# Kernel tuning notes

Measured on AMD Instinct MI355X. Metric: run time of the kernel, lower is better.

## Reference

```python
import jax, jax.numpy as jnp
import numpy as np

BATCH, DIN, HID = 32768, 64, 1024


def setup_inputs() -> dict:
    key = jax.random.key(0)
    ks = jax.random.split(key, 8)
    s_in = 1.0 / np.sqrt(DIN)
    s_h = 1.0 / np.sqrt(HID)
    return {
        "z": jax.random.normal(ks[0], (BATCH, DIN), dtype=jnp.float32),
        # Hamiltonian net: DIN -> HID -> HID -> 1
        "W1": jax.random.normal(ks[1], (DIN, HID), dtype=jnp.float32) * s_in,
        "b1": jnp.zeros((HID,), jnp.float32),
        "W2": jax.random.normal(ks[2], (HID, HID), dtype=jnp.float32) * s_h,
        "b2": jnp.zeros((HID,), jnp.float32),
        "W3": jax.random.normal(ks[3], (HID, 1), dtype=jnp.float32) * s_h,
        "b3": jnp.zeros((1,), jnp.float32),
        # Forcing net: DIN -> HID -> DIN
        "Wf1": jax.random.normal(ks[4], (DIN, HID), dtype=jnp.float32) * s_in,
        "bf1": jnp.zeros((HID,), jnp.float32),
        "Wf2": jax.random.normal(ks[5], (HID, DIN), dtype=jnp.float32) * s_h,
        "bf2": jnp.zeros((DIN,), jnp.float32),
    }


def reference(z, W1, b1, W2, b2, W3, b3, Wf1, bf1, Wf2, bf2):
    def H_sum(zz):
        h1 = jnp.tanh(zz @ W1 + b1)          # [B, HID]
        h2 = jnp.tanh(h1 @ W2 + b2)          # [B, HID]
        return jnp.sum(h2 @ W3 + b3)         # scalar (sum of H over batch)

    gradH = jax.grad(H_sum)(z)               # [B, DIN]
    dim = z.shape[1] // 2
    # symplectic combine: dq/dt = dH/dp, dp/dt = -dH/dq
    hnn_term = jnp.concatenate([gradH[:, dim:], -gradH[:, :dim]], axis=-1)
    forcing_term = jnp.tanh(z @ Wf1 + bf1) @ Wf2 + bf2  # [B, DIN]
    return hnn_term + forcing_term
```

## Files before the change

kernel.cpp:

```cpp
#include <hip/hip_runtime.h>


typedef __attribute__((ext_vector_type(8))) short s16x8;
typedef __attribute__((ext_vector_type(4))) float f32x4;
typedef unsigned short u16;

#define DEVFN static __device__ __forceinline__

constexpr int DIN = 64;
constexpr int HID = 1024;

DEVFN u16 f2bf(float f) {
  unsigned u = __builtin_bit_cast(unsigned, f);
  u += 0x7fffu + ((u >> 16) & 1u);
  return (u16)(u >> 16);
}
DEVFN float bf2f(u16 h) {
  unsigned u = ((unsigned)h) << 16;
  return __builtin_bit_cast(float, u);
}
DEVFN float fast_tanh(float x) {
  float e = __builtin_amdgcn_exp2f(x * 2.8853900817779268f);
  return 1.0f - 2.0f * __builtin_amdgcn_rcpf(e + 1.0f);
}
DEVFN f32x4 mfma16(s16x8 a, s16x8 b, f32x4 c) {
  return __builtin_amdgcn_mfma_f32_16x16x32_bf16(a, b, c, 0, 0, 0);
}

#define GLOAD16(g, l) __builtin_amdgcn_global_load_lds( \
    (const __attribute__((address_space(1))) unsigned int*)(const void*)(g), \
    (__attribute__((address_space(3))) unsigned int*)(void*)(l), 16, 0, 0)

__global__ __launch_bounds__(256) void k0_prep(
    const float* __restrict__ W2, const float* __restrict__ W1,
    const float* __restrict__ Wf1, const float* __restrict__ Wf2,
    u16* __restrict__ W2tp, u16* __restrict__ W2c,
    u16* __restrict__ W1p, u16* __restrict__ Wf1p,
    u16* __restrict__ W1s, u16* __restrict__ Wf2p) {
  __shared__ u16 tl[64 * 65];
  const int bi = blockIdx.x >> 4, bj = blockIdx.x & 15;
  const int tid = threadIdx.x;
#pragma unroll
  for (int i = 0; i < 16; ++i) {
    int idx = i * 256 + tid;
    int r = idx >> 6, c = idx & 63;
    float v = W2[(size_t)(bi * 64 + r) * 1024 + bj * 64 + c];
    u16 b = f2bf(v);
    W2c[(size_t)(bi * 64 + r) * 1024 + bj * 64 + c] = b;
    tl[r * 65 + c] = b;
  }
  __syncthreads();
#pragma unroll
  for (int i = 0; i < 16; ++i) {
    int idx = i * 256 + tid;
    int r = idx >> 6, c = idx & 63;
    W2tp[(size_t)(bj * 64 + r) * 1024 + bi * 64 + c] = tl[c * 65 + r];
  }
  int id = blockIdx.x * 256 + tid;
  int n = id >> 6, k = id & 63;
  W1p[id]  = f2bf(W1[k * HID + n]);
  Wf1p[id] = f2bf(Wf1[k * HID + n]);
  int nn = id >> 10, kk2 = id & 1023;
  float s = (nn < 32) ? 1.f : -1.f;
  W1s[id]  = f2bf(s * W1[((nn + 32) & 63) * HID + kk2]);
  Wf2p[id] = f2bf(Wf2[kk2 * DIN + nn]);
}

__global__ __launch_bounds__(256) void k1_h1(const float* z, const u16* Wp,
                                             const float* b, u16* o) {
  __shared__ __align__(16) u16 zl[64 * 72];
  const int tid = threadIdx.x;
  const int lane = tid & 63, w = tid >> 6;
  const int nb = blockIdx.x & 7, mb = blockIdx.x >> 3;
  const size_t m0 = (size_t)mb * 64;
  const int n0 = nb * 128;
#pragma unroll
  for (int c = 0; c < 4; ++c) {
    int i4 = c * 256 + tid;
    int row = i4 >> 4, col4 = (i4 & 15) * 4;
    f32x4 v = *reinterpret_cast<const f32x4*>(z + (m0 + row) * DIN + col4);
    u16* d = zl + row * 72 + col4;
    d[0] = f2bf(v[0]); d[1] = f2bf(v[1]); d[2] = f2bf(v[2]); d[3] = f2bf(v[3]);
  }
  __syncthreads();
  f32x4 acc[8] = {};
#pragma unroll
  for (int kk = 0; kk < 2; ++kk) {
    const int karr = kk * 32 + ((lane >> 4) << 3);
    s16x8 a = *reinterpret_cast<const s16x8*>(zl + (16 * w + (lane & 15)) * 72 + karr);
#pragma unroll
    for (int fn = 0; fn < 8; ++fn) {
      int n = n0 + fn * 16 + (lane & 15);
      s16x8 bb = *reinterpret_cast<const s16x8*>(Wp + (size_t)n * 64 + karr);
      acc[fn] = mfma16(a, bb, acc[fn]);
    }
  }
#pragma unroll
  for (int fn = 0; fn < 8; ++fn) {
    int n = n0 + fn * 16 + (lane & 15);
    float bias = b[n];
#pragma unroll
    for (int j = 0; j < 4; ++j) {
      size_t m = m0 + 16 * w + ((lane >> 4) << 2) + j;
      o[m * HID + n] = f2bf(fast_tanh(acc[fn][j] + bias));
    }
  }
}

template <int MODE>
__global__ __launch_bounds__(512, 2) void k23_gemm(
    const u16* __restrict__ A, const u16* __restrict__ Bp,
    const float* __restrict__ b2, const float* __restrict__ W3,
    const u16* __restrict__ h1in, u16* __restrict__ outb) {
  extern __shared__ u16 lds[];
  const int tid = threadIdx.x;
  const int lane = tid & 63, w = tid >> 6;
  const int wr = w >> 2, wc = w & 3;
  const int xcd = blockIdx.x & 7, local = blockIdx.x >> 3;
  const size_t m0 = (size_t)(xcd * 16 + (local >> 2)) * 256;
  const int n0 = (local & 3) * 256;

  const u16* gpa[4]; const u16* gpb[4]; int lo[4];
#pragma unroll
  for (int c = 0; c < 4; ++c) {
    int idx = c * 512 + tid, row = idx >> 3, cg = idx & 7;
    int sc = (cg ^ (row & 7)) << 3;
    gpa[c] = A + (m0 + row) * 1024 + sc;
    gpb[c] = Bp + (size_t)(n0 + row) * 1024 + sc;
    lo[c] = idx * 8;
  }
#define STAGE_A(B_, T_) { _Pragma("unroll") for (int c = 0; c < 4; ++c) \
    GLOAD16(gpa[c] + (T_) * 64, lds + (B_) * 32768 + lo[c]); }
#define STAGE_B(B_, T_) { _Pragma("unroll") for (int c = 0; c < 4; ++c) \
    GLOAD16(gpb[c] + (T_) * 64, lds + (B_) * 32768 + 16384 + lo[c]); }

  const int swz = (lane & 7) << 3;
  int aoff[8], boff[4];
#pragma unroll
  for (int i = 0; i < 8; ++i)
    aoff[i] = (wr * 128 + i * 16 + (lane & 15)) * 64 + ((lane >> 4) << 3);
#pragma unroll
  for (int j = 0; j < 4; ++j)
    boff[j] = (wc * 64 + j * 16 + (lane & 15)) * 64 + ((lane >> 4) << 3);

  f32x4 acc[8][4] = {};

#define PHASE(B_, KK_) { \
    s16x8 af[8], bf[4]; \
    _Pragma("unroll") for (int i = 0; i < 8; ++i) \
      af[i] = *reinterpret_cast<const s16x8*>(lds + (B_) * 32768 + ((aoff[i] + (KK_) * 32) ^ swz)); \
    _Pragma("unroll") for (int j = 0; j < 4; ++j) \
      bf[j] = *reinterpret_cast<const s16x8*>(lds + (B_) * 32768 + 16384 + ((boff[j] + (KK_) * 32) ^ swz)); \
    __builtin_amdgcn_s_setprio(1); \
    _Pragma("unroll") for (int i = 0; i < 8; ++i) { \
      _Pragma("unroll") for (int j = 0; j < 4; ++j) \
        acc[i][j] = mfma16(af[i], bf[j], acc[i][j]); } \
    __builtin_amdgcn_s_setprio(0); }

  STAGE_A(0, 0); STAGE_B(0, 0);
  for (int t = 0; t < 15; ++t) {
    const int cur = t & 1, nxt = cur ^ 1;
    STAGE_A(nxt, t + 1);
    asm volatile("s_waitcnt vmcnt(4)" ::: "memory");
    __builtin_amdgcn_s_barrier();
    asm volatile("" ::: "memory");
    PHASE(cur, 0);
    STAGE_B(nxt, t + 1);
    PHASE(cur, 1);
    asm volatile("" ::: "memory");
    __builtin_amdgcn_s_barrier();
    asm volatile("" ::: "memory");
  }
  asm volatile("s_waitcnt vmcnt(0)" ::: "memory");
  __builtin_amdgcn_s_barrier();
  asm volatile("" ::: "memory");
  PHASE(1, 0);
  PHASE(1, 1);
  asm volatile("" ::: "memory");
  __builtin_amdgcn_s_barrier();
  asm volatile("" ::: "memory");

  const int wbase = w * 8192;
  float b2v[4], w3v[4];
  if (MODE == 0) {
#pragma unroll
    for (int j = 0; j < 4; ++j) {
      int n = n0 + wc * 64 + j * 16 + (lane & 15);
      b2v[j] = b2[n]; w3v[j] = W3[n];
    }
  }
#pragma unroll
  for (int h = 0; h < 2; ++h) {
    if (h == 1) asm volatile("s_waitcnt lgkmcnt(0)" ::: "memory");
#pragma unroll
    for (int ip = 0; ip < 4; ++ip) {
#pragma unroll
      for (int j = 0; j < 4; ++j) {
#pragma unroll
        for (int r = 0; r < 4; ++r) {
          float v = acc[h * 4 + ip][j][r];
          u16 o;
          if (MODE == 0) {
            float tt = fast_tanh(v + b2v[j]);
            o = f2bf(w3v[j] * (1.f - tt * tt));
          } else {
            o = f2bf(v);
          }
          int lr = ip * 16 + ((lane >> 4) << 2) + r;
          lds[wbase + lr * 64 + j * 16 + (lane & 15)] = o;
        }
      }
    }
#pragma unroll
    for (int r8 = 0; r8 < 8; ++r8) {
      int lr = r8 * 8 + (lane >> 3), c8 = (lane & 7) * 8;
      s16x8 vv = *reinterpret_cast<const s16x8*>(lds + wbase + lr * 64 + c8);
      size_t grow = m0 + wr * 128 + h * 64 + lr;
      int gcol = n0 + wc * 64 + c8;
      if (MODE == 1) {
        s16x8 hh = *reinterpret_cast<const s16x8*>(h1in + grow * 1024 + gcol);
#pragma unroll
        for (int e = 0; e < 8; ++e) {
          float hv = bf2f((u16)hh[e]);
          vv[e] = (short)f2bf(bf2f((u16)vv[e]) * (1.f - hv * hv));
        }
      }
      *reinterpret_cast<s16x8*>(outb + grow * 1024 + gcol) = vv;
    }
  }
#undef STAGE_A
#undef STAGE_B
#undef PHASE
}

__global__ __launch_bounds__(512) void k4_gemm(
    const u16* __restrict__ gp1, const u16* __restrict__ f1,
    const u16* __restrict__ W1s, const u16* __restrict__ Wf2p,
    const float* __restrict__ bf2, float* __restrict__ out) {
  __shared__ __align__(16) u16 Ab[2][2][4096];
  __shared__ __align__(16) u16 Bb[2][2][4096];
  const int tid = threadIdx.x;
  const int w8 = tid >> 6, lane = tid & 63;
  const int grp = w8 >> 2, w = w8 & 3;
  const int gt = tid & 255;
  const int lr = lane & 15, g = lane >> 4;
  const size_t m0 = (size_t)blockIdx.x * 64;
  const u16* asrc = grp ? f1 : gp1;
  const u16* bsrc = grp ? Wf2p : W1s;

  int aoffs[2], boffs[2], lo[2];
#pragma unroll
  for (int c = 0; c < 2; ++c) {
    int idx = c * 256 + gt;
    int row = idx >> 3, cg = idx & 7;
    aoffs[c] = (int)((m0 + row) * 1024) + ((cg ^ (row & 7)) << 3);
    boffs[c] = row * 1024 + ((cg ^ (row & 7)) << 3);
    lo[c] = idx * 8;
  }
#define K4STAGE(B_, T_) { const int ko_ = (T_) * 64; \
    _Pragma("unroll") for (int c = 0; c < 2; ++c) { \
      GLOAD16(asrc + aoffs[c] + ko_, Ab[grp][B_] + lo[c]); \
      GLOAD16(bsrc + boffs[c] + ko_, Bb[grp][B_] + lo[c]); } }

  const int arow = w * 16 + lr;
  int afr[2], bfr[2][4];
#pragma unroll
  for (int kkl = 0; kkl < 2; ++kkl) {
    afr[kkl] = arow * 64 + ((kkl * 32 + g * 8) ^ ((arow & 7) << 3));
#pragma unroll
    for (int fn = 0; fn < 4; ++fn) {
      int br = fn * 16 + lr;
      bfr[kkl][fn] = br * 64 + ((kkl * 32 + g * 8) ^ ((br & 7) << 3));
    }
  }

  f32x4 acc[4] = {};
#define K4MM(BUF_) { \
    _Pragma("unroll") for (int kkl = 0; kkl < 2; ++kkl) { \
      s16x8 a = *reinterpret_cast<const s16x8*>(Ab[grp][BUF_] + afr[kkl]); \
      _Pragma("unroll") for (int fn = 0; fn < 4; ++fn) { \
        s16x8 b = *reinterpret_cast<const s16x8*>(Bb[grp][BUF_] + bfr[kkl][fn]); \
        acc[fn] = mfma16(a, b, acc[fn]); } } }
#define TBAR() { asm volatile("" ::: "memory"); __builtin_amdgcn_s_barrier(); asm volatile("" ::: "memory"); }

  K4STAGE(0, 0);
  for (int t = 0; t < 15; ++t) {
    K4STAGE((t + 1) & 1, t + 1);
    asm volatile("s_waitcnt vmcnt(4)" ::: "memory");
    TBAR();
    K4MM(t & 1);
    TBAR();
  }
  asm volatile("s_waitcnt vmcnt(0)" ::: "memory");
  TBAR();
  K4MM(1);

  __syncthreads();
  float* red = (float*)&Ab[0][0][0];
  if (grp == 1) {
#pragma unroll
    for (int fn = 0; fn < 4; ++fn)
#pragma unroll
      for (int j = 0; j < 4; ++j)
        red[(fn * 4 + j) * 256 + gt] = acc[fn][j];
  }
  __syncthreads();
  if (grp == 0) {
#pragma unroll
    for (int fn = 0; fn < 4; ++fn) {
      int n = fn * 16 + lr;
      float bias = bf2[n];
#pragma unroll
      for (int j = 0; j < 4; ++j) {
        float v = acc[fn][j] + red[(fn * 4 + j) * 256 + gt] + bias;
        size_t m = m0 + w * 16 + g * 4 + j;
        out[m * DIN + n] = v;
      }
    }
  }
#undef K4STAGE
#undef K4MM
#undef TBAR
}

extern "C" void kernel_launch(void* const* d_in, const int* in_sizes, int n_in,
                              void* d_out, int out_size, void* d_ws, size_t ws_size,
                              hipStream_t stream) {
  const float* z   = (const float*)d_in[0];
  const float* W1  = (const float*)d_in[1];
  const float* b1  = (const float*)d_in[2];
  const float* W2  = (const float*)d_in[3];
  const float* b2  = (const float*)d_in[4];
  const float* W3  = (const float*)d_in[5];
  const float* Wf1 = (const float*)d_in[7];
  const float* bf1 = (const float*)d_in[8];
  const float* Wf2 = (const float*)d_in[9];
  const float* bf2 = (const float*)d_in[10];

  char* ws = (char*)d_ws;
  u16* W1p  = (u16*)(ws + 0);
  u16* Wf1p = (u16*)(ws + 131072);
  u16* W2tp = (u16*)(ws + 262144);
  u16* W2c  = (u16*)(ws + 2359296);
  u16* W1s  = (u16*)(ws + 4456448);
  u16* Wf2p = (u16*)(ws + 4587520);
  u16* h1   = (u16*)(ws + 4718592);
  u16* gp2  = (u16*)(ws + 4718592 + 67108864ull);
  float* out = (float*)d_out;

  k0_prep<<<256, 256, 0, stream>>>(W2, W1, Wf1, Wf2, W2tp, W2c, W1p, Wf1p, W1s, Wf2p);
  k1_h1<<<4096, 256, 0, stream>>>(z, W1p, b1, h1);
  k23_gemm<0><<<512, 512, 131072, stream>>>(h1, W2tp, b2, W3, nullptr, gp2);
  k23_gemm<1><<<512, 512, 131072, stream>>>(gp2, W2c, nullptr, nullptr, h1, h1);
  k1_h1<<<4096, 256, 0, stream>>>(z, Wf1p, bf1, gp2);
  k4_gemm<<<512, 512, 0, stream>>>(h1, gp2, W1s, Wf2p, bf2, out);
}
```

Measured before the change: 251.3 us.

## Split GEMM main loop into four barrier-separated sub-phases with staggered loads

Restructures the double-buffered GEMM main loop into four sub-phases per K-step. Each sub-phase reads half of the A fragments plus the B fragments, issues a quarter of the next tile's global-to-LDS loads, and runs 16 MFMAs, with extra barriers in between. This halves the A-fragment register footprint, which frees registers, and interleaves loads more finely with compute in a ping-pong style schedule. In exchange it roughly triples the number of barriers per iteration, which can stall waves if they are not balanced.

```diff
diff --git a/kernel.cpp b/kernel.cpp
--- a/kernel.cpp
+++ b/kernel.cpp
@@ -129,10 +129,14 @@
     gpb[c] = Bp + (size_t)(n0 + row) * 1024 + sc;
     lo[c] = idx * 8;
   }
-#define STAGE_A(B_, T_) { _Pragma("unroll") for (int c = 0; c < 4; ++c) \
-    GLOAD16(gpa[c] + (T_) * 64, lds + (B_) * 32768 + lo[c]); }
-#define STAGE_B(B_, T_) { _Pragma("unroll") for (int c = 0; c < 4; ++c) \
-    GLOAD16(gpb[c] + (T_) * 64, lds + (B_) * 32768 + 16384 + lo[c]); }
+#define STAGE_H(B_, T_, H_) { \
+    if ((H_) < 2) { \
+      GLOAD16(gpa[(H_) * 2]     + (T_) * 64, lds + (B_) * 32768 + lo[(H_) * 2]); \
+      GLOAD16(gpa[(H_) * 2 + 1] + (T_) * 64, lds + (B_) * 32768 + lo[(H_) * 2 + 1]); \
+    } else { \
+      GLOAD16(gpb[((H_) - 2) * 2]     + (T_) * 64, lds + (B_) * 32768 + 16384 + lo[((H_) - 2) * 2]); \
+      GLOAD16(gpb[((H_) - 2) * 2 + 1] + (T_) * 64, lds + (B_) * 32768 + 16384 + lo[((H_) - 2) * 2 + 1]); \
+    } }
 
   const int swz = (lane & 7) << 3;
   int aoff[8], boff[4];
@@ -144,41 +148,58 @@
     boff[j] = (wc * 64 + j * 16 + (lane & 15)) * 64 + ((lane >> 4) << 3);
 
   f32x4 acc[8][4] = {};
-
-#define PHASE(B_, KK_) { \
-    s16x8 af[8], bf[4]; \
-    _Pragma("unroll") for (int i = 0; i < 8; ++i) \
-      af[i] = *reinterpret_cast<const s16x8*>(lds + (B_) * 32768 + ((aoff[i] + (KK_) * 32) ^ swz)); \
-    _Pragma("unroll") for (int j = 0; j < 4; ++j) \
-      bf[j] = *reinterpret_cast<const s16x8*>(lds + (B_) * 32768 + 16384 + ((boff[j] + (KK_) * 32) ^ swz)); \
-    __builtin_amdgcn_s_setprio(1); \
-    _Pragma("unroll") for (int i = 0; i < 8; ++i) { \
+  s16x8 af[4], bf[4];
+
+#define RDB(B_, KK_) { _Pragma("unroll") for (int j = 0; j < 4; ++j) \
+    bf[j] = *reinterpret_cast<const s16x8*>(lds + (B_) * 32768 + 16384 + ((boff[j] + (KK_) * 32) ^ swz)); }
+#define RDA(B_, MH_, KK_) { _Pragma("unroll") for (int i = 0; i < 4; ++i) \
+    af[i] = *reinterpret_cast<const s16x8*>(lds + (B_) * 32768 + ((aoff[(MH_) * 4 + i] + (KK_) * 32) ^ swz)); }
+#define MM16(MH_) { __builtin_amdgcn_s_setprio(1); \
+    _Pragma("unroll") for (int i = 0; i < 4; ++i) { \
       _Pragma("unroll") for (int j = 0; j < 4; ++j) \
-        acc[i][j] = mfma16(af[i], bf[j], acc[i][j]); } \
+        acc[(MH_) * 4 + i][j] = mfma16(af[i], bf[j], acc[(MH_) * 4 + i][j]); } \
     __builtin_amdgcn_s_setprio(0); }
-
-  STAGE_A(0, 0); STAGE_B(0, 0);
+#define BAR() { asm volatile("" ::: "memory"); __builtin_amdgcn_s_barrier(); asm volatile("" ::: "memory"); }
+
+  STAGE_H(0, 0, 0); STAGE_H(0, 0, 1); STAGE_H(0, 0, 2); STAGE_H(0, 0, 3);
   for (int t = 0; t < 15; ++t) {
     const int cur = t & 1, nxt = cur ^ 1;
-    STAGE_A(nxt, t + 1);
-    asm volatile("s_waitcnt vmcnt(4)" ::: "memory");
-    __builtin_amdgcn_s_barrier();
-    asm volatile("" ::: "memory");
-    PHASE(cur, 0);
-    STAGE_B(nxt, t + 1);
-    PHASE(cur, 1);
-    asm volatile("" ::: "memory");
-    __builtin_amdgcn_s_barrier();
-    asm volatile("" ::: "memory");
+    STAGE_H(nxt, t + 1, 0);
+    asm volatile("s_waitcnt vmcnt(2)" ::: "memory");
+    BAR();
+    RDB(cur, 0); RDA(cur, 0, 0);
+    MM16(0);
+    BAR();
+    RDA(cur, 1, 0);
+    STAGE_H(nxt, t + 1, 1);
+    BAR();
+    MM16(1);
+    BAR();
+    RDB(cur, 1); RDA(cur, 0, 1);
+    STAGE_H(nxt, t + 1, 2);
+    BAR();
+    MM16(0);
+    BAR();
+    RDA(cur, 1, 1);
+    STAGE_H(nxt, t + 1, 3);
+    BAR();
+    MM16(1);
+    BAR();
   }
   asm volatile("s_waitcnt vmcnt(0)" ::: "memory");
-  __builtin_amdgcn_s_barrier();
-  asm volatile("" ::: "memory");
-  PHASE(1, 0);
-  PHASE(1, 1);
-  asm volatile("" ::: "memory");
-  __builtin_amdgcn_s_barrier();
-  asm volatile("" ::: "memory");
+  BAR();
+  RDB(1, 0); RDA(1, 0, 0);
+  MM16(0);
+  BAR();
+  RDA(1, 1, 0);
+  MM16(1);
+  BAR();
+  RDB(1, 1); RDA(1, 0, 1);
+  MM16(0);
+  BAR();
+  RDA(1, 1, 1);
+  MM16(1);
+  BAR();
 
   const int wbase = w * 8192;
   float b2v[4], w3v[4];
@@ -228,9 +249,11 @@
       *reinterpret_cast<s16x8*>(outb + grow * 1024 + gcol) = vv;
     }
   }
-#undef STAGE_A
-#undef STAGE_B
-#undef PHASE
+#undef STAGE_H
+#undef RDB
+#undef RDA
+#undef MM16
+#undef BAR
 }
 
 __global__ __launch_bounds__(512) void k4_gemm(
```

Measured after the change: 253.1 us. Within noise of the previous version (+0.7%).
